# Optimization experiments

Hardware: AMD Instinct MI355X
Metric: run time of the kernel (lower is better)

Reference implementation:

```python
import jax, jax.numpy as jnp
import numpy as np

N_NODES = 100000
N_EDGES = 1600000
D_FEAT = 128
HIDDEN = 128
N_CLASSES = 40


def setup_inputs() -> dict:
    key = jax.random.key(0)
    ks = jax.random.split(key, 8)
    s = 1.0 / np.sqrt(HIDDEN)
    return {
        "x": jax.random.normal(ks[0], (N_NODES, D_FEAT), dtype=jnp.float32),
        "edge_index": jax.random.randint(ks[1], (2, N_EDGES), 0, N_NODES, dtype=jnp.int64),
        "w1a": jax.random.normal(ks[2], (D_FEAT, HIDDEN), dtype=jnp.float32) * s,
        "b1a": jnp.zeros((HIDDEN,), dtype=jnp.float32),
        "w1b": jax.random.normal(ks[3], (HIDDEN, HIDDEN), dtype=jnp.float32) * s,
        "b1b": jnp.zeros((HIDDEN,), dtype=jnp.float32),
        "w2a": jax.random.normal(ks[4], (HIDDEN, HIDDEN), dtype=jnp.float32) * s,
        "b2a": jnp.zeros((HIDDEN,), dtype=jnp.float32),
        "w2b": jax.random.normal(ks[5], (HIDDEN, HIDDEN), dtype=jnp.float32) * s,
        "b2b": jnp.zeros((HIDDEN,), dtype=jnp.float32),
        "wfc": jax.random.normal(ks[6], (HIDDEN, N_CLASSES), dtype=jnp.float32) * s,
        "bfc": jnp.zeros((N_CLASSES,), dtype=jnp.float32),
    }


def _gin_conv(x, src, dst, wa, ba, wb, bb):
    # sum-aggregate neighbor features: agg[i] = sum_{(j->i) in E} x[j]
    agg = jax.ops.segment_sum(x[src], dst, num_segments=N_NODES)
    h = x + agg  # eps = 0 (PyG GINConv default)
    h = jax.nn.relu(h @ wa + ba)
    return h @ wb + bb


def reference(x, edge_index, w1a, b1a, w1b, b1b, w2a, b2a, w2b, b2b, wfc, bfc):
    src, dst = edge_index[0], edge_index[1]
    h = jax.nn.relu(_gin_conv(x, src, dst, w1a, b1a, w1b, b1b))
    # dropout is identity at inference
    h = jax.nn.relu(_gin_conv(h, src, dst, w2a, b2a, w2b, b2b))
    logits = h @ wfc + bfc
    return jax.nn.log_softmax(logits, axis=1)
```

## Files before the change

kernel.cpp:

```cpp
#include <hip/hip_runtime.h>
#include <hip/hip_bf16.h>

#define NNODES 100000
#define NEDGES 1600000
#define DF 128
#define NC 40
#define NCP 48
#define NB 196
#define CH 4096
#define MLP_BLOCKS 256
#define MLP_WAVES (MLP_BLOCKS * 4)
#define ZROW NNODES

typedef __bf16 bf16x8 __attribute__((ext_vector_type(8)));
typedef float f32x4 __attribute__((ext_vector_type(4)));
typedef float f32x2 __attribute__((ext_vector_type(2)));

__device__ __forceinline__ unsigned short f2bf(float f) {
    unsigned int u = __builtin_bit_cast(unsigned int, f);
    u = (u + 0x7FFFu + ((u >> 16) & 1u)) >> 16;
    return (unsigned short)u;
}
__device__ __forceinline__ float bf2f(unsigned short s) {
    unsigned int u = ((unsigned int)s) << 16;
    return __builtin_bit_cast(float, u);
}
__device__ __forceinline__ float bfLo(unsigned int u) {
    return __builtin_bit_cast(float, u << 16);
}
__device__ __forceinline__ float bfHi(unsigned int u) {
    return __builtin_bit_cast(float, u & 0xFFFF0000u);
}
__device__ __forceinline__ f32x2 up2(unsigned int u) {
    return (f32x2){bfLo(u), bfHi(u)};
}

__global__ void k_detect(const unsigned int* __restrict__ ei32,
                         const unsigned int* __restrict__ x32,
                         int* __restrict__ flags,
                         int* __restrict__ binCnt) {
    __shared__ unsigned int rOr[256];
    __shared__ int rCnt[256];
    for (int i = threadIdx.x; i < NB; i += 256) binCnt[i] = 0;
    unsigned int o = 0; int c = 0;
    for (int i = threadIdx.x; i < 1024; i += 256) o |= ei32[2 * i + 1];
    for (int i = threadIdx.x; i < 4096; i += 256) {
        unsigned int e = (x32[i] >> 7) & 0xFFu;
        c += (e >= 100u && e <= 140u) ? 1 : 0;
    }
    rOr[threadIdx.x] = o; rCnt[threadIdx.x] = c;
    __syncthreads();
    for (int s = 128; s; s >>= 1) {
        if ((int)threadIdx.x < s) {
            rOr[threadIdx.x] |= rOr[threadIdx.x + s];
            rCnt[threadIdx.x] += rCnt[threadIdx.x + s];
        }
        __syncthreads();
    }
    if (threadIdx.x == 0) {
        flags[0] = (rOr[0] == 0u) ? 1 : 0;
        flags[1] = (rCnt[0] > 2457) ? 1 : 0;
    }
}

__device__ __forceinline__ int ldIdx(const void* ei, int flag64, int i) {
    return flag64 ? (int)((const long long*)ei)[i] : ((const int*)ei)[i];
}

__global__ __launch_bounds__(256) void k_cvt_feat(const void* __restrict__ src,
                                                  const int* __restrict__ flags,
                                                  unsigned short* __restrict__ dst) {
    int i = blockIdx.x * 256 + threadIdx.x;
    if (flags[1]) {
        ((uint4*)dst)[i] = ((const uint4*)src)[i];
    } else {
        uint4 a = ((const uint4*)src)[2 * i];
        uint4 b = ((const uint4*)src)[2 * i + 1];
        auto pk = [](unsigned int lo, unsigned int hi) -> unsigned int {
            return ((unsigned int)f2bf(__builtin_bit_cast(float, hi)) << 16) |
                   f2bf(__builtin_bit_cast(float, lo));
        };
        uint4 r;
        r.x = pk(a.x, a.y);
        r.y = pk(a.z, a.w);
        r.z = pk(b.x, b.y);
        r.w = pk(b.z, b.w);
        ((uint4*)dst)[i] = r;
    }
}

__global__ __launch_bounds__(256) void k_wprep(const void* w1a, const void* w1b,
                                               const void* w2a, const void* w2b,
                                               const void* wfc,
                                               const void* b1a, const void* b1b,
                                               const void* b2a, const void* b2b,
                                               const void* bfc,
                                               const int* __restrict__ flags,
                                               unsigned short* __restrict__ wAll,
                                               float* __restrict__ bAll,
                                               unsigned short* __restrict__ pad0,
                                               unsigned short* __restrict__ pad1) {
    int idx = blockIdx.x * 256 + threadIdx.x;
    int bf = flags[1];
    auto ldf = [&](const void* p, int i) -> float {
        return bf ? bf2f(((const unsigned short*)p)[i]) : ((const float*)p)[i];
    };
    if (idx < 65536) {
        int wi = idx >> 14, r = idx & 16383;
        int n = r >> 7, k = r & 127;
        const void* s = (wi == 0) ? w1a : (wi == 1) ? w1b : (wi == 2) ? w2a : w2b;
        wAll[idx] = f2bf(ldf(s, k * 128 + n));
    } else if (idx < 65536 + NCP * 128) {
        int r = idx - 65536;
        int n = r >> 7, k = r & 127;
        wAll[idx] = (n < NC) ? f2bf(ldf(wfc, k * NC + n)) : (unsigned short)0;
    } else if (idx < 65536 + NCP * 128 + 512 + NC) {
        int r = idx - (65536 + NCP * 128);
        const void* s; int i;
        if (r < 128)      { s = b1a; i = r; }
        else if (r < 256) { s = b1b; i = r - 128; }
        else if (r < 384) { s = b2a; i = r - 256; }
        else if (r < 512) { s = b2b; i = r - 384; }
        else              { s = bfc; i = r - 512; }
        bAll[r] = ldf(s, i);
    } else if (idx < 65536 + NCP * 128 + 512 + NC + 256) {
        pad0[idx - (65536 + NCP * 128 + 512 + NC)] = 0;
    } else if (idx < 65536 + NCP * 128 + 512 + NC + 512) {
        pad1[idx - (65536 + NCP * 128 + 512 + NC + 256)] = 0;
    }
}

__global__ __launch_bounds__(256) void k_bincount(const void* __restrict__ ei,
                                                  const int* __restrict__ flags,
                                                  int* __restrict__ binCnt) {
    __shared__ int l[NB];
    int t = threadIdx.x;
    int f64 = flags[0];
    for (int i = t; i < NB; i += 256) l[i] = 0;
    __syncthreads();
    int base = blockIdx.x * CH;
#pragma unroll
    for (int k = 0; k < CH / 256; k++) {
        int e = base + k * 256 + t;
        if (e < NEDGES) atomicAdd(&l[ldIdx(ei, f64, NEDGES + e) >> 9], 1);
    }
    __syncthreads();
    for (int i = t; i < NB; i += 256)
        if (l[i]) atomicAdd(&binCnt[i], l[i]);
}

__global__ __launch_bounds__(256) void k_binscan(const int* __restrict__ binCnt,
                                                 int* __restrict__ binOfs,
                                                 int* __restrict__ binCur) {
    __shared__ int sh[256];
    int t = threadIdx.x;
    int v = (t < NB) ? binCnt[t] : 0;
    sh[t] = v;
    __syncthreads();
    for (int off = 1; off < 256; off <<= 1) {
        int x = (t >= off) ? sh[t - off] : 0;
        __syncthreads();
        sh[t] += x;
        __syncthreads();
    }
    if (t < NB) {
        binOfs[t + 1] = sh[t];
        binCur[t] = sh[t] - v;
    }
    if (t == 0) binOfs[0] = 0;
}

__global__ __launch_bounds__(256) void k_binscatter(const void* __restrict__ ei,
                                                    const int* __restrict__ flags,
                                                    int* __restrict__ binCur,
                                                    int2* __restrict__ ebin) {
    __shared__ int lcnt[NB], lbase[NB], lofs[NB];
    int t = threadIdx.x;
    int f64 = flags[0];
    for (int i = t; i < NB; i += 256) lcnt[i] = 0;
    __syncthreads();
    int base = blockIdx.x * CH;
    int2 ed[CH / 256];
    int bn[CH / 256];
#pragma unroll
    for (int k = 0; k < CH / 256; k++) {
        int e = base + k * 256 + t;
        if (e < NEDGES) {
            ed[k].x = ldIdx(ei, f64, e);
            ed[k].y = ldIdx(ei, f64, NEDGES + e);
            bn[k] = ed[k].y >> 9;
            atomicAdd(&lcnt[bn[k]], 1);
        } else bn[k] = -1;
    }
    __syncthreads();
    if (t < NB) {
        int c = lcnt[t];
        lbase[t] = c ? atomicAdd(&binCur[t], c) : 0;
        lofs[t] = 0;
    }
    __syncthreads();
#pragma unroll
    for (int k = 0; k < CH / 256; k++) {
        if (bn[k] >= 0) {
            int p = lbase[bn[k]] + atomicAdd(&lofs[bn[k]], 1);
            ebin[p] = ed[k];
        }
    }
}

__global__ __launch_bounds__(256) void k_binfill(const int2* __restrict__ ebin,
                                                 const int* __restrict__ binOfs,
                                                 int* __restrict__ rowptr,
                                                 int* __restrict__ perm) {
    __shared__ int deg[512], lptr[512], ssum[256];
    int b = blockIdx.x, t = threadIdx.x;
    int n0 = b << 9;
    int nn = NNODES - n0; if (nn > 512) nn = 512;
    int e0 = binOfs[b], e1 = binOfs[b + 1];
    deg[t] = 0; deg[t + 256] = 0;
    __syncthreads();
    for (int e = e0 + t; e < e1; e += 256)
        atomicAdd(&deg[ebin[e].y - n0], 1);
    __syncthreads();
    int d0 = deg[2 * t], d1 = deg[2 * t + 1];
    int s = d0 + d1;
    ssum[t] = s;
    __syncthreads();
    for (int off = 1; off < 256; off <<= 1) {
        int x = (t >= off) ? ssum[t - off] : 0;
        __syncthreads();
        ssum[t] += x;
        __syncthreads();
    }
    int ex = ssum[t] - s;
    lptr[2 * t] = ex;
    lptr[2 * t + 1] = ex + d0;
    if (2 * t < nn)     rowptr[n0 + 2 * t] = e0 + ex;
    if (2 * t + 1 < nn) rowptr[n0 + 2 * t + 1] = e0 + ex + d0;
    if (b == NB - 1 && t == 0) rowptr[NNODES] = e1;
    deg[2 * t] = 0; deg[2 * t + 1] = 0;
    __syncthreads();
    for (int e = e0 + t; e < e1; e += 256) {
        int2 ed = ebin[e];
        int d = ed.y - n0;
        int pos = e0 + lptr[d] + atomicAdd(&deg[d], 1);
        perm[pos] = ed.x;
    }
}

__device__ __forceinline__ void accu(f32x2* acc, uint4 u) {
    acc[0] += up2(u.x);
    acc[1] += up2(u.y);
    acc[2] += up2(u.z);
    acc[3] += up2(u.w);
}

template <int S>
__device__ __forceinline__ void gslots(const int* __restrict__ perm, const uint4* __restrict__ F,
                                       int j, int je, int g, int c, f32x2* acc) {
    int pm[S];
#pragma unroll
    for (int k = 0; k < S; k++) pm[k] = perm[j + 4 * k + g];
#pragma unroll
    for (int k = 0; k < S; k++)
        if (j + 4 * k + g >= je) pm[k] = ZROW;
    uint4 u[S];
#pragma unroll
    for (int k = 0; k < S; k++) u[k] = F[pm[k] * 16 + c];
#pragma unroll
    for (int k = 0; k < S; k++) accu(acc, u[k]);
}

__global__ __launch_bounds__(256) void k_gather(const unsigned short* __restrict__ feat,
                                                const unsigned short* __restrict__ x,
                                                const int* __restrict__ rowptr,
                                                const int* __restrict__ perm,
                                                unsigned short* __restrict__ out) {
    int wave = threadIdx.x >> 6, lane = threadIdx.x & 63;
    int i = blockIdx.x * 4 + wave;
    int g = lane >> 4, c = lane & 15;
    const uint4* F = (const uint4*)feat;

    uint4 xv = ((const uint4*)x)[i * 16 + c];
    int jb = rowptr[i], je = rowptr[i + 1];

    f32x2 acc[4];
#pragma unroll
    for (int k = 0; k < 4; k++) acc[k] = (f32x2){0.f, 0.f};

    int j = jb;
    while (je - j > 24) {
        int s0 = perm[j + g], s1 = perm[j + 4 + g];
        int s2 = perm[j + 8 + g], s3 = perm[j + 12 + g];
        uint4 u0 = F[s0 * 16 + c];
        uint4 u1 = F[s1 * 16 + c];
        uint4 u2 = F[s2 * 16 + c];
        uint4 u3 = F[s3 * 16 + c];
        accu(acc, u0); accu(acc, u1); accu(acc, u2); accu(acc, u3);
        j += 16;
    }
    int deg = je - j;
    if (deg > 16)      gslots<6>(perm, F, j, je, g, c, acc);
    else if (deg > 8)  gslots<4>(perm, F, j, je, g, c, acc);
    else if (deg > 0)  gslots<2>(perm, F, j, je, g, c, acc);

#pragma unroll
    for (int k = 0; k < 4; k++) {
        acc[k][0] += __shfl_xor(acc[k][0], 16);
        acc[k][1] += __shfl_xor(acc[k][1], 16);
        acc[k][0] += __shfl_xor(acc[k][0], 32);
        acc[k][1] += __shfl_xor(acc[k][1], 32);
    }

    acc[0] += up2(xv.x);
    acc[1] += up2(xv.y);
    acc[2] += up2(xv.z);
    acc[3] += up2(xv.w);

    if (g == 0) {
        uint4 r;
        r.x = ((unsigned int)f2bf(acc[0][1]) << 16) | f2bf(acc[0][0]);
        r.y = ((unsigned int)f2bf(acc[1][1]) << 16) | f2bf(acc[1][0]);
        r.z = ((unsigned int)f2bf(acc[2][1]) << 16) | f2bf(acc[2][0]);
        r.w = ((unsigned int)f2bf(acc[3][1]) << 16) | f2bf(acc[3][0]);
        ((uint4*)out)[i * 16 + c] = r;
    }
}

template <bool DOFC>
__global__ __launch_bounds__(256, 1) void k_mlp_rb(const unsigned short* __restrict__ A,
                                                   const unsigned short* __restrict__ WaT,
                                                   const float* __restrict__ ba,
                                                   const unsigned short* __restrict__ WbT,
                                                   const float* __restrict__ bb,
                                                   const unsigned short* __restrict__ WfcT,
                                                   const float* __restrict__ bfc,
                                                   const int* __restrict__ flags,
                                                   unsigned short* __restrict__ outH,
                                                   void* __restrict__ outFC) {
    __shared__ __align__(16) unsigned short smem[4 * 2176];
    int wave = threadIdx.x >> 6, lane = threadIdx.x & 63;
    int gw = blockIdx.x * 4 + wave;
    int m = lane & 15, quad = lane >> 4;
    unsigned short* T = smem + wave * 2176;

    bf16x8 wa[8][4], wb[8][4];
#pragma unroll
    for (int nt = 0; nt < 8; nt++) {
        const unsigned short* Ba = WaT + (nt * 16 + m) * DF + quad * 8;
        const unsigned short* Bb = WbT + (nt * 16 + m) * DF + quad * 8;
#pragma unroll
        for (int ks = 0; ks < 4; ks++) {
            wa[nt][ks] = *(const bf16x8*)(Ba + ks * 32);
            wb[nt][ks] = *(const bf16x8*)(Bb + ks * 32);
        }
    }
    float bva[8], bvb[8];
#pragma unroll
    for (int nt = 0; nt < 8; nt++) { bva[nt] = ba[nt * 16 + m]; bvb[nt] = bb[nt * 16 + m]; }

    bf16x8 wf[3][4];
    float fv0 = 0.f, fv1 = 0.f, fv2 = 0.f;
    bool valid2 = (m < 8);
    int obf = 0;
    if (DOFC) {
#pragma unroll
        for (int nt = 0; nt < 3; nt++) {
            const unsigned short* Bf = WfcT + (nt * 16 + m) * DF + quad * 8;
#pragma unroll
            for (int ks = 0; ks < 4; ks++) wf[nt][ks] = *(const bf16x8*)(Bf + ks * 32);
        }
        fv0 = bfc[m]; fv1 = bfc[16 + m];
        fv2 = valid2 ? bfc[32 + m] : 0.f;
        obf = flags[1];
    }

    auto ladr = [](int row, int col) -> int {
        int chunk = (col >> 3) ^ ((row >> 3) << 2);
        return row * 136 + chunk * 8 + (col & 7);
    };

    for (int tile = gw; tile < NNODES / 16; tile += MLP_WAVES) {
        int r0 = tile * 16;
        const unsigned short* Ab = A + (r0 + m) * DF + quad * 8;
        bf16x8 a[4];
#pragma unroll
        for (int ks = 0; ks < 4; ks++) a[ks] = *(const bf16x8*)(Ab + ks * 32);

        f32x4 acc[8];
#pragma unroll
        for (int nt = 0; nt < 8; nt++) acc[nt] = (f32x4){0.f, 0.f, 0.f, 0.f};
#pragma unroll
        for (int nt = 0; nt < 8; nt++)
#pragma unroll
            for (int ks = 0; ks < 4; ks++)
                acc[nt] = __builtin_amdgcn_mfma_f32_16x16x32_bf16(a[ks], wa[nt][ks], acc[nt], 0, 0, 0);

#pragma unroll
        for (int nt = 0; nt < 8; nt++)
#pragma unroll
            for (int reg = 0; reg < 4; reg++) {
                float v = acc[nt][reg] + bva[nt];
                if (v < 0.f) v = 0.f;
                T[ladr(quad * 4 + reg, nt * 16 + m)] = f2bf(v);
            }

        bf16x8 a2[4];
#pragma unroll
        for (int ks = 0; ks < 4; ks++) {
            int chunk = (ks * 4 + quad) ^ ((m >> 3) << 2);
            a2[ks] = *(const bf16x8*)&T[m * 136 + chunk * 8];
        }
#pragma unroll
        for (int nt = 0; nt < 8; nt++) acc[nt] = (f32x4){0.f, 0.f, 0.f, 0.f};
#pragma unroll
        for (int nt = 0; nt < 8; nt++)
#pragma unroll
            for (int ks = 0; ks < 4; ks++)
                acc[nt] = __builtin_amdgcn_mfma_f32_16x16x32_bf16(a2[ks], wb[nt][ks], acc[nt], 0, 0, 0);

        if (!DOFC) {
#pragma unroll
            for (int nt = 0; nt < 8; nt++) {
                int col = nt * 16 + m;
#pragma unroll
                for (int reg = 0; reg < 4; reg++) {
                    int row = r0 + quad * 4 + reg;
                    float v = acc[nt][reg] + bvb[nt];
                    if (v < 0.f) v = 0.f;
                    outH[row * DF + col] = f2bf(v);
                }
            }
        } else {
#pragma unroll
            for (int nt = 0; nt < 8; nt++)
#pragma unroll
                for (int reg = 0; reg < 4; reg++) {
                    float v = acc[nt][reg] + bvb[nt];
                    if (v < 0.f) v = 0.f;
                    T[ladr(quad * 4 + reg, nt * 16 + m)] = f2bf(v);
                }
            bf16x8 a3[4];
#pragma unroll
            for (int ks = 0; ks < 4; ks++) {
                int chunk = (ks * 4 + quad) ^ ((m >> 3) << 2);
                a3[ks] = *(const bf16x8*)&T[m * 136 + chunk * 8];
            }
            f32x4 fa[3];
#pragma unroll
            for (int nt = 0; nt < 3; nt++) fa[nt] = (f32x4){0.f, 0.f, 0.f, 0.f};
#pragma unroll
            for (int nt = 0; nt < 3; nt++)
#pragma unroll
                for (int ks = 0; ks < 4; ks++)
                    fa[nt] = __builtin_amdgcn_mfma_f32_16x16x32_bf16(a3[ks], wf[nt][ks], fa[nt], 0, 0, 0);

#pragma unroll
            for (int reg = 0; reg < 4; reg++) {
                float v0 = fa[0][reg] + fv0;
                float v1 = fa[1][reg] + fv1;
                float v2 = valid2 ? (fa[2][reg] + fv2) : -3.0e38f;
                float mx = fmaxf(fmaxf(v0, v1), v2);
#pragma unroll
                for (int off = 1; off < 16; off <<= 1) mx = fmaxf(mx, __shfl_xor(mx, off, 16));
                float e = __expf(v0 - mx) + __expf(v1 - mx) + (valid2 ? __expf(v2 - mx) : 0.f);
#pragma unroll
                for (int off = 1; off < 16; off <<= 1) e += __shfl_xor(e, off, 16);
                float l = mx + __logf(e);
                int row = r0 + quad * 4 + reg;
                if (obf) {
                    unsigned short* o = (unsigned short*)outFC + row * NC;
                    o[m] = f2bf(v0 - l);
                    o[16 + m] = f2bf(v1 - l);
                    if (valid2) o[32 + m] = f2bf(v2 - l);
                } else {
                    float* o = (float*)outFC + row * NC;
                    o[m] = v0 - l;
                    o[16 + m] = v1 - l;
                    if (valid2) o[32 + m] = v2 - l;
                }
            }
        }
    }
}

extern "C" void kernel_launch(void* const* d_in, const int* in_sizes, int n_in,
                              void* d_out, int out_size, void* d_ws, size_t ws_size,
                              hipStream_t stream) {
    const void* x   = d_in[0];
    const void* ei  = d_in[1];
    const void* w1a = d_in[2];
    const void* b1a = d_in[3];
    const void* w1b = d_in[4];
    const void* b1b = d_in[5];
    const void* w2a = d_in[6];
    const void* b2a = d_in[7];
    const void* w2b = d_in[8];
    const void* b2b = d_in[9];
    const void* wfc = d_in[10];
    const void* bfc = d_in[11];

    char* ws = (char*)d_ws;
    size_t off = 0;
    auto alloc = [&](size_t bytes) {
        void* p = ws + off;
        off += (bytes + 255) & ~(size_t)255;
        return p;
    };
    unsigned short* B0    = (unsigned short*)alloc((size_t)(NNODES + 1) * DF * 2);
    unsigned short* B1    = (unsigned short*)alloc((size_t)(NNODES + 1) * DF * 2);
    int2*           ebin  = (int2*)alloc((size_t)NEDGES * 8);
    int*            perm  = (int*)alloc((size_t)(NEDGES + 64) * 4);
    int*            rowptr= (int*)alloc((size_t)(NNODES + 1) * 4);
    int*            binCnt= (int*)alloc(NB * 4);
    int*            binOfs= (int*)alloc((NB + 1) * 4);
    int*            binCur= (int*)alloc(NB * 4);
    int*            flags = (int*)alloc(256);
    unsigned short* wAll  = (unsigned short*)alloc((4 * 16384 + NCP * 128) * 2);
    float*          bAll  = (float*)alloc((512 + NC) * 4);

    unsigned short* w1aT = wAll;
    unsigned short* w1bT = wAll + 16384;
    unsigned short* w2aT = wAll + 32768;
    unsigned short* w2bT = wAll + 49152;
    unsigned short* wfcT = wAll + 65536;
    float* b1af = bAll;
    float* b1bf = bAll + 128;
    float* b2af = bAll + 256;
    float* b2bf = bAll + 384;
    float* bfcf = bAll + 512;

    k_detect<<<1, 256, 0, stream>>>((const unsigned int*)ei, (const unsigned int*)x, flags, binCnt);
    k_cvt_feat<<<NNODES * DF / (256 * 8), 256, 0, stream>>>(x, flags, B0);

    int wprepN = 4 * 16384 + NCP * 128 + 512 + NC + 512;
    k_wprep<<<(wprepN + 255) / 256, 256, 0, stream>>>(w1a, w1b, w2a, w2b, wfc,
                                                      b1a, b1b, b2a, b2b, bfc,
                                                      flags, wAll, bAll,
                                                      B0 + (size_t)NNODES * DF,
                                                      B1 + (size_t)NNODES * DF);

    int nEB = (NEDGES + CH - 1) / CH;
    k_bincount<<<nEB, 256, 0, stream>>>(ei, flags, binCnt);
    k_binscan<<<1, 256, 0, stream>>>(binCnt, binOfs, binCur);
    k_binscatter<<<nEB, 256, 0, stream>>>(ei, flags, binCur, ebin);
    k_binfill<<<NB, 256, 0, stream>>>(ebin, binOfs, rowptr, perm);

    const int gatherGrid = NNODES / 4;

    k_gather<<<gatherGrid, 256, 0, stream>>>(B0, B0, rowptr, perm, B1);
    k_mlp_rb<false><<<MLP_BLOCKS, 256, 0, stream>>>(B1, w1aT, b1af, w1bT, b1bf,
                                                    nullptr, nullptr, flags, B0, nullptr);

    k_gather<<<gatherGrid, 256, 0, stream>>>(B0, B0, rowptr, perm, B1);
    k_mlp_rb<true><<<MLP_BLOCKS, 256, 0, stream>>>(B1, w2aT, b2af, w2bT, b2bf,
                                                   wfcT, bfcf, flags, nullptr, d_out);
}
```

Before: 367.1 us.

## Stage second-layer and FC weights in LDS to double MLP occupancy; fuse prep kernels

The MLP kernel no longer keeps the Wb and Wfc weight fragments in registers. It stages them once per block into XOR-swizzled shared memory and reads them per tile, which frees enough registers to raise launch bounds to 2 blocks per CU and double the MLP grid. The scratch tile layout moves to the same unpadded swizzle. Separately, the feature-conversion and weight-prep kernels are merged into one launch to save a kernel dispatch. The cost is extra LDS traffic on every tile, plus a per-block weight copy and barrier.

```diff
diff --git a/kernel.cpp b/kernel.cpp
--- a/kernel.cpp
+++ b/kernel.cpp
@@ -8,9 +8,10 @@
 #define NCP 48
 #define NB 196
 #define CH 4096
-#define MLP_BLOCKS 256
+#define MLP_BLOCKS 512
 #define MLP_WAVES (MLP_BLOCKS * 4)
 #define ZROW NNODES
+#define CVT_BLOCKS 6250
 
 typedef __bf16 bf16x8 __attribute__((ext_vector_type(8)));
 typedef float f32x4 __attribute__((ext_vector_type(4)));
@@ -67,41 +68,41 @@
     return flag64 ? (int)((const long long*)ei)[i] : ((const int*)ei)[i];
 }
 
-__global__ __launch_bounds__(256) void k_cvt_feat(const void* __restrict__ src,
-                                                  const int* __restrict__ flags,
-                                                  unsigned short* __restrict__ dst) {
-    int i = blockIdx.x * 256 + threadIdx.x;
-    if (flags[1]) {
-        ((uint4*)dst)[i] = ((const uint4*)src)[i];
-    } else {
-        uint4 a = ((const uint4*)src)[2 * i];
-        uint4 b = ((const uint4*)src)[2 * i + 1];
-        auto pk = [](unsigned int lo, unsigned int hi) -> unsigned int {
-            return ((unsigned int)f2bf(__builtin_bit_cast(float, hi)) << 16) |
-                   f2bf(__builtin_bit_cast(float, lo));
-        };
-        uint4 r;
-        r.x = pk(a.x, a.y);
-        r.y = pk(a.z, a.w);
-        r.z = pk(b.x, b.y);
-        r.w = pk(b.z, b.w);
-        ((uint4*)dst)[i] = r;
-    }
-}
-
-__global__ __launch_bounds__(256) void k_wprep(const void* w1a, const void* w1b,
-                                               const void* w2a, const void* w2b,
-                                               const void* wfc,
-                                               const void* b1a, const void* b1b,
-                                               const void* b2a, const void* b2b,
-                                               const void* bfc,
-                                               const int* __restrict__ flags,
-                                               unsigned short* __restrict__ wAll,
-                                               float* __restrict__ bAll,
-                                               unsigned short* __restrict__ pad0,
-                                               unsigned short* __restrict__ pad1) {
-    int idx = blockIdx.x * 256 + threadIdx.x;
+__global__ __launch_bounds__(256) void k_prep(const void* __restrict__ src,
+                                              const void* w1a, const void* w1b,
+                                              const void* w2a, const void* w2b,
+                                              const void* wfc,
+                                              const void* b1a, const void* b1b,
+                                              const void* b2a, const void* b2b,
+                                              const void* bfc,
+                                              const int* __restrict__ flags,
+                                              unsigned short* __restrict__ dst,
+                                              unsigned short* __restrict__ wAll,
+                                              float* __restrict__ bAll,
+                                              unsigned short* __restrict__ pad0,
+                                              unsigned short* __restrict__ pad1) {
     int bf = flags[1];
+    if (blockIdx.x < CVT_BLOCKS) {
+        int i = blockIdx.x * 256 + threadIdx.x;
+        if (bf) {
+            ((uint4*)dst)[i] = ((const uint4*)src)[i];
+        } else {
+            uint4 a = ((const uint4*)src)[2 * i];
+            uint4 b = ((const uint4*)src)[2 * i + 1];
+            auto pk = [](unsigned int lo, unsigned int hi) -> unsigned int {
+                return ((unsigned int)f2bf(__builtin_bit_cast(float, hi)) << 16) |
+                       f2bf(__builtin_bit_cast(float, lo));
+            };
+            uint4 r;
+            r.x = pk(a.x, a.y);
+            r.y = pk(a.z, a.w);
+            r.z = pk(b.x, b.y);
+            r.w = pk(b.z, b.w);
+            ((uint4*)dst)[i] = r;
+        }
+        return;
+    }
+    int idx = (blockIdx.x - CVT_BLOCKS) * 256 + threadIdx.x;
     auto ldf = [&](const void* p, int i) -> float {
         return bf ? bf2f(((const unsigned short*)p)[i]) : ((const float*)p)[i];
     };
@@ -328,7 +329,7 @@
 }
 
 template <bool DOFC>
-__global__ __launch_bounds__(256, 1) void k_mlp_rb(const unsigned short* __restrict__ A,
+__global__ __launch_bounds__(256, 2) void k_mlp_rb(const unsigned short* __restrict__ A,
                                                    const unsigned short* __restrict__ WaT,
                                                    const float* __restrict__ ba,
                                                    const unsigned short* __restrict__ WbT,
@@ -338,46 +339,49 @@
                                                    const int* __restrict__ flags,
                                                    unsigned short* __restrict__ outH,
                                                    void* __restrict__ outFC) {
-    __shared__ __align__(16) unsigned short smem[4 * 2176];
+    __shared__ __align__(16) unsigned short sWb[16384];
+    __shared__ __align__(16) unsigned short sWf[DOFC ? 6144 : 16];
+    __shared__ __align__(16) unsigned short sT[4][2048];
+
     int wave = threadIdx.x >> 6, lane = threadIdx.x & 63;
     int gw = blockIdx.x * 4 + wave;
     int m = lane & 15, quad = lane >> 4;
-    unsigned short* T = smem + wave * 2176;
-
-    bf16x8 wa[8][4], wb[8][4];
+    unsigned short* T = sT[wave];
+
+    for (int idx = threadIdx.x; idx < 16384; idx += 256) {
+        int n = idx >> 7, k = idx & 127;
+        sWb[(n << 7) | (((k >> 3) ^ (n & 15)) << 3) | (k & 7)] = WbT[idx];
+    }
+    if (DOFC) {
+        for (int idx = threadIdx.x; idx < 6144; idx += 256) {
+            int n = idx >> 7, k = idx & 127;
+            sWf[(n << 7) | (((k >> 3) ^ (n & 15)) << 3) | (k & 7)] = WfcT[idx];
+        }
+    }
+
+    bf16x8 wa[8][4];
 #pragma unroll
     for (int nt = 0; nt < 8; nt++) {
         const unsigned short* Ba = WaT + (nt * 16 + m) * DF + quad * 8;
-        const unsigned short* Bb = WbT + (nt * 16 + m) * DF + quad * 8;
-#pragma unroll
-        for (int ks = 0; ks < 4; ks++) {
+#pragma unroll
+        for (int ks = 0; ks < 4; ks++)
             wa[nt][ks] = *(const bf16x8*)(Ba + ks * 32);
-            wb[nt][ks] = *(const bf16x8*)(Bb + ks * 32);
-        }
     }
     float bva[8], bvb[8];
 #pragma unroll
     for (int nt = 0; nt < 8; nt++) { bva[nt] = ba[nt * 16 + m]; bvb[nt] = bb[nt * 16 + m]; }
-
-    bf16x8 wf[3][4];
     float fv0 = 0.f, fv1 = 0.f, fv2 = 0.f;
     bool valid2 = (m < 8);
     int obf = 0;
     if (DOFC) {
-#pragma unroll
-        for (int nt = 0; nt < 3; nt++) {
-            const unsigned short* Bf = WfcT + (nt * 16 + m) * DF + quad * 8;
-#pragma unroll
-            for (int ks = 0; ks < 4; ks++) wf[nt][ks] = *(const bf16x8*)(Bf + ks * 32);
-        }
         fv0 = bfc[m]; fv1 = bfc[16 + m];
         fv2 = valid2 ? bfc[32 + m] : 0.f;
         obf = flags[1];
     }
+    __syncthreads();
 
     auto ladr = [](int row, int col) -> int {
-        int chunk = (col >> 3) ^ ((row >> 3) << 2);
-        return row * 136 + chunk * 8 + (col & 7);
+        return (row << 7) | (((col >> 3) ^ (row & 15)) << 3) | (col & 7);
     };
 
     for (int tile = gw; tile < NNODES / 16; tile += MLP_WAVES) {
@@ -407,17 +411,20 @@
 
         bf16x8 a2[4];
 #pragma unroll
-        for (int ks = 0; ks < 4; ks++) {
-            int chunk = (ks * 4 + quad) ^ ((m >> 3) << 2);
-            a2[ks] = *(const bf16x8*)&T[m * 136 + chunk * 8];
+        for (int ks = 0; ks < 4; ks++)
+            a2[ks] = *(const bf16x8*)&T[(m << 7) | ((((ks << 2) + quad) ^ m) << 3)];
+#pragma unroll
+        for (int nt = 0; nt < 8; nt++) acc[nt] = (f32x4){0.f, 0.f, 0.f, 0.f};
+#pragma unroll
+        for (int nt = 0; nt < 8; nt++) {
+            bf16x8 wbf[4];
+#pragma unroll
+            for (int ks = 0; ks < 4; ks++)
+                wbf[ks] = *(const bf16x8*)&sWb[((nt * 16 + m) << 7) | ((((ks << 2) + quad) ^ m) << 3)];
+#pragma unroll
+            for (int ks = 0; ks < 4; ks++)
+                acc[nt] = __builtin_amdgcn_mfma_f32_16x16x32_bf16(a2[ks], wbf[ks], acc[nt], 0, 0, 0);
         }
-#pragma unroll
-        for (int nt = 0; nt < 8; nt++) acc[nt] = (f32x4){0.f, 0.f, 0.f, 0.f};
-#pragma unroll
-        for (int nt = 0; nt < 8; nt++)
-#pragma unroll
-            for (int ks = 0; ks < 4; ks++)
-                acc[nt] = __builtin_amdgcn_mfma_f32_16x16x32_bf16(a2[ks], wb[nt][ks], acc[nt], 0, 0, 0);
 
         if (!DOFC) {
 #pragma unroll
@@ -442,18 +449,21 @@
                 }
             bf16x8 a3[4];
 #pragma unroll
-            for (int ks = 0; ks < 4; ks++) {
-                int chunk = (ks * 4 + quad) ^ ((m >> 3) << 2);
-                a3[ks] = *(const bf16x8*)&T[m * 136 + chunk * 8];
+            for (int ks = 0; ks < 4; ks++)
+                a3[ks] = *(const bf16x8*)&T[(m << 7) | ((((ks << 2) + quad) ^ m) << 3)];
+            f32x4 fa[3];
+#pragma unroll
+            for (int nt = 0; nt < 3; nt++) fa[nt] = (f32x4){0.f, 0.f, 0.f, 0.f};
+#pragma unroll
+            for (int nt = 0; nt < 3; nt++) {
+                bf16x8 wff[4];
+#pragma unroll
+                for (int ks = 0; ks < 4; ks++)
+                    wff[ks] = *(const bf16x8*)&sWf[((nt * 16 + m) << 7) | ((((ks << 2) + quad) ^ m) << 3)];
+#pragma unroll
+                for (int ks = 0; ks < 4; ks++)
+                    fa[nt] = __builtin_amdgcn_mfma_f32_16x16x32_bf16(a3[ks], wff[ks], fa[nt], 0, 0, 0);
             }
-            f32x4 fa[3];
-#pragma unroll
-            for (int nt = 0; nt < 3; nt++) fa[nt] = (f32x4){0.f, 0.f, 0.f, 0.f};
-#pragma unroll
-            for (int nt = 0; nt < 3; nt++)
-#pragma unroll
-                for (int ks = 0; ks < 4; ks++)
-                    fa[nt] = __builtin_amdgcn_mfma_f32_16x16x32_bf16(a3[ks], wf[nt][ks], fa[nt], 0, 0, 0);
 
 #pragma unroll
             for (int reg = 0; reg < 4; reg++) {
@@ -531,14 +541,13 @@
     float* bfcf = bAll + 512;
 
     k_detect<<<1, 256, 0, stream>>>((const unsigned int*)ei, (const unsigned int*)x, flags, binCnt);
-    k_cvt_feat<<<NNODES * DF / (256 * 8), 256, 0, stream>>>(x, flags, B0);
-
     int wprepN = 4 * 16384 + NCP * 128 + 512 + NC + 512;
-    k_wprep<<<(wprepN + 255) / 256, 256, 0, stream>>>(w1a, w1b, w2a, w2b, wfc,
-                                                      b1a, b1b, b2a, b2b, bfc,
-                                                      flags, wAll, bAll,
-                                                      B0 + (size_t)NNODES * DF,
-                                                      B1 + (size_t)NNODES * DF);
+    int prepGrid = CVT_BLOCKS + (wprepN + 255) / 256;
+    k_prep<<<prepGrid, 256, 0, stream>>>(x, w1a, w1b, w2a, w2b, wfc,
+                                         b1a, b1b, b2a, b2b, bfc,
+                                         flags, B0, wAll, bAll,
+                                         B0 + (size_t)NNODES * DF,
+                                         B1 + (size_t)NNODES * DF);
 
     int nEB = (NEDGES + CH - 1) / CH;
     k_bincount<<<nEB, 256, 0, stream>>>(ei, flags, binCnt);
```

Result: slower. 400.0 us (+9.0%).
